# Performance work log

Hardware: AMD Instinct MI355X
Metric: run time of the kernel (lower is better)

The kernel has to match this reference:

```python
import jax, jax.numpy as jnp
import numpy as np

B, C, H, W_ = 4, 256, 64, 64
INTER = 128

def conv1x1(x, w, b):
    # x: [B,C,H,W], w: [O,C], b: [O] -> [B,O,H,W]
    return jnp.einsum('bchw,oc->bohw', x, w) + b[None, :, None, None]

def setup_inputs() -> dict:
    key = jax.random.key(0)
    ks = jax.random.split(key, 5)
    s_in = 1.0 / np.sqrt(C)
    s_mid = 1.0 / np.sqrt(INTER)
    return {
        'x': jax.random.normal(ks[0], (B, C, H, W_), dtype=jnp.float32),
        'w_g': jax.random.normal(ks[1], (INTER, C), dtype=jnp.float32) * s_in,
        'b_g': jnp.zeros((INTER,), dtype=jnp.float32),
        'w_theta': jax.random.normal(ks[2], (INTER, C), dtype=jnp.float32) * s_in,
        'b_theta': jnp.zeros((INTER,), dtype=jnp.float32),
        'w_phi': jax.random.normal(ks[3], (INTER, C), dtype=jnp.float32) * s_in,
        'b_phi': jnp.zeros((INTER,), dtype=jnp.float32),
        'w_out': jax.random.normal(ks[4], (C, INTER), dtype=jnp.float32) * s_mid,
        'b_out': jnp.zeros((C,), dtype=jnp.float32),
    }

def reference(x, w_g, b_g, w_theta, b_theta, w_phi, b_phi, w_out, b_out):
    b, c, h, w = x.shape
    n = h * w
    # 1x1 conv projections, flatten spatial dims to N tokens
    g_x = conv1x1(x, w_g, b_g).reshape(b, INTER, n).transpose(0, 2, 1)      # [B,N,I]
    theta_x = conv1x1(x, w_theta, b_theta).reshape(b, INTER, n).transpose(0, 2, 1)  # [B,N,I]
    phi_x = conv1x1(x, w_phi, b_phi).reshape(b, INTER, n)                   # [B,I,N]
    f = jnp.einsum('bni,bim->bnm', theta_x, phi_x)                          # [B,N,N]
    f_div_C = jax.nn.softmax(f, axis=-1)
    y = jnp.einsum('bnm,bmi->bni', f_div_C, g_x)                            # [B,N,I]
    y = y.transpose(0, 2, 1).reshape(b, INTER, h, w)
    W_y = conv1x1(y, w_out, b_out)                                          # [B,C,H,W]
    return W_y + x
```

## Files before the change

kernel.cpp:

```cpp
#include <hip/hip_runtime.h>

#define BB 4
#define CC 256
#define NN 4096
#define II 128
#define NSPLIT 4
#define KVH (NN / NSPLIT)
#define NT (KVH / 64)
#define LOG2E 1.4426950408889634f

typedef float f32x4 __attribute__((ext_vector_type(4)));
typedef _Float16 f16x8 __attribute__((ext_vector_type(8)));

static __device__ __forceinline__ unsigned short f2h(float f) {
    _Float16 h = (_Float16)f;
    return __builtin_bit_cast(unsigned short, h);
}
static __device__ __forceinline__ float h2f(unsigned short s) {
    return (float)__builtin_bit_cast(_Float16, s);
}
static __device__ __forceinline__ unsigned int pack2h(float a, float b) {
    return (unsigned int)f2h(a) | ((unsigned int)f2h(b) << 16);
}
static __device__ __forceinline__ unsigned int cvt2h(float a, float b) {
    return __builtin_bit_cast(unsigned int, __builtin_amdgcn_cvt_pkrtz(a, b));
}
#define M3(a, b, c) fmaxf(fmaxf((a), (b)), (c))

__global__ __launch_bounds__(256) void proj_kernel(
    const float* __restrict__ x,
    const float* __restrict__ w_th, const float* __restrict__ b_th,
    const float* __restrict__ w_ph, const float* __restrict__ b_ph,
    const float* __restrict__ w_g,  const float* __restrict__ b_g,
    const float* __restrict__ w_out,
    unsigned short* __restrict__ Qb, unsigned short* __restrict__ Kb,
    unsigned short* __restrict__ Vt, unsigned short* __restrict__ Wo)
{
    __shared__ char lds[24576];
    unsigned short* wl = (unsigned short*)lds;
    unsigned short* xl = (unsigned short*)(lds + 16384);

    int tid = threadIdx.x;
    int w = tid >> 6, l = tid & 63, g = l >> 4, cl = l & 15;
    int mat = blockIdx.z, b = blockIdx.y, n0 = blockIdx.x * 64;
    const float* wp = (mat == 0) ? w_th : (mat == 1) ? w_ph : w_g;
    const float* bp = (mat == 0) ? b_th : (mat == 1) ? b_ph : b_g;

    f32x4 acc[2][4];
    #pragma unroll
    for (int it = 0; it < 2; ++it)
        #pragma unroll
        for (int nt = 0; nt < 4; ++nt) acc[it][nt] = (f32x4){0.f, 0.f, 0.f, 0.f};

    const float* xb = x + (size_t)b * CC * NN;
    int c2 = tid >> 3, nch = tid & 7;

    for (int c0 = 0; c0 < CC; c0 += 64) {
        __syncthreads();
        #pragma unroll
        for (int r = 0; r < 4; ++r) {
            int idx = r * 256 + tid;
            int row = idx >> 3, ch = idx & 7;
            const float* src = wp + row * CC + c0 + ch * 8;
            float4 a = *(const float4*)src;
            float4 bq = *(const float4*)(src + 4);
            union { unsigned int u[4]; uint4 q; } pk;
            pk.u[0] = pack2h(a.x, a.y);  pk.u[1] = pack2h(a.z, a.w);
            pk.u[2] = pack2h(bq.x, bq.y); pk.u[3] = pack2h(bq.z, bq.w);
            *(uint4*)((char*)wl + row * 128 + ((ch ^ (row & 7)) << 4)) = pk.q;
        }
        {
            const float* xsrc = xb + (size_t)(c0 + c2 * 2) * NN + n0 + nch * 8;
            float4 x00 = *(const float4*)xsrc;
            float4 x01 = *(const float4*)(xsrc + 4);
            float4 x10 = *(const float4*)(xsrc + NN);
            float4 x11 = *(const float4*)(xsrc + NN + 4);
            float lo[8] = {x00.x, x00.y, x00.z, x00.w, x01.x, x01.y, x01.z, x01.w};
            float hi[8] = {x10.x, x10.y, x10.z, x10.w, x11.x, x11.y, x11.z, x11.w};
            #pragma unroll
            for (int t = 0; t < 8; ++t) {
                int n = nch * 8 + t;
                *(unsigned int*)((char*)xl + n * 128 + ((c2 * 4) ^ ((n & 7) << 4))) = pack2h(lo[t], hi[t]);
            }
        }
        __syncthreads();
        #pragma unroll
        for (int kc = 0; kc < 2; ++kc) {
            f16x8 af[2], bf[4];
            #pragma unroll
            for (int it = 0; it < 2; ++it) {
                int row = w * 32 + it * 16 + cl;
                af[it] = *(const f16x8*)((const char*)wl + row * 128 + (((kc * 4 + g) ^ (row & 7)) << 4));
            }
            #pragma unroll
            for (int nt = 0; nt < 4; ++nt) {
                int row = nt * 16 + cl;
                bf[nt] = *(const f16x8*)((const char*)xl + row * 128 + (((kc * 4 + g) ^ (row & 7)) << 4));
            }
            #pragma unroll
            for (int it = 0; it < 2; ++it)
                #pragma unroll
                for (int nt = 0; nt < 4; ++nt)
                    acc[it][nt] = __builtin_amdgcn_mfma_f32_16x16x32_f16(af[it], bf[nt], acc[it][nt], 0, 0, 0);
        }
    }

    float bv[2][4];
    #pragma unroll
    for (int it = 0; it < 2; ++it)
        #pragma unroll
        for (int r = 0; r < 4; ++r) bv[it][r] = bp[w * 32 + it * 16 + 4 * g + r];
    float scale = (mat == 0) ? LOG2E : 1.0f;

    __syncthreads();
    if (mat < 2) {
        unsigned short* pk = (unsigned short*)lds;
        #pragma unroll
        for (int it = 0; it < 2; ++it)
            #pragma unroll
            for (int nt = 0; nt < 4; ++nt)
                #pragma unroll
                for (int r = 0; r < 4; r += 2) {
                    int n = nt * 16 + cl;
                    int i = w * 32 + it * 16 + 4 * g + r;
                    unsigned int v = pack2h((acc[it][nt][r] + bv[it][r]) * scale,
                                            (acc[it][nt][r + 1] + bv[it][r + 1]) * scale);
                    *(unsigned int*)((char*)pk + n * 256 + ((i * 2) ^ ((n & 7) << 4))) = v;
                }
        __syncthreads();
        unsigned short* out = (mat == 0) ? Qb : Kb;
        #pragma unroll
        for (int r = 0; r < 4; ++r) {
            int idx = r * 256 + tid;
            int n = idx >> 4, seg = idx & 15;
            uint4 q = *(const uint4*)((const char*)pk + n * 256 + ((seg << 4) ^ ((n & 7) << 4)));
            *(uint4*)(out + (size_t)(b * NN + n0 + n) * II + seg * 8) = q;
        }
    } else {
        unsigned short* pk = (unsigned short*)lds;
        #pragma unroll
        for (int it = 0; it < 2; ++it)
            #pragma unroll
            for (int nt = 0; nt < 4; ++nt)
                #pragma unroll
                for (int r = 0; r < 4; ++r) {
                    int i = w * 32 + it * 16 + 4 * g + r;
                    int n = nt * 16 + cl;
                    *(unsigned short*)((char*)pk + i * 128 + ((n * 2) ^ ((i & 7) << 4))) =
                        f2h(acc[it][nt][r] + bv[it][r]);
                }
        __syncthreads();
        #pragma unroll
        for (int r = 0; r < 4; ++r) {
            int idx = r * 256 + tid;
            int i = idx >> 3, seg = idx & 7;
            uint4 q = *(const uint4*)((const char*)pk + i * 128 + ((seg << 4) ^ ((i & 7) << 4)));
            *(uint4*)(Vt + (size_t)(b * II + i) * NN + n0 + seg * 8) = q;
        }
        if (blockIdx.x == 0) {
            #pragma unroll
            for (int r = 0; r < 16; ++r) {
                int idx = (r * 256 + tid) * 8;
                float4 a = *(const float4*)(w_out + idx);
                float4 b4 = *(const float4*)(w_out + idx + 4);
                union { unsigned int u[4]; uint4 q; } pw;
                pw.u[0] = pack2h(a.x, a.y);   pw.u[1] = pack2h(a.z, a.w);
                pw.u[2] = pack2h(b4.x, b4.y); pw.u[3] = pack2h(b4.z, b4.w);
                *(uint4*)&Wo[idx] = pw.q;
            }
        }
    }
}

__global__ __launch_bounds__(256, 2) void attn_kernel(
    const unsigned short* __restrict__ Qb,
    const unsigned short* __restrict__ Kb,
    const unsigned short* __restrict__ Vb,
    unsigned short* __restrict__ Yp,
    float2* __restrict__ ML)
{
    __shared__ unsigned short Ks[2][64 * 128];
    __shared__ unsigned short Vs[2][128 * 64];

    int tid = threadIdx.x;
    int w = tid >> 6, l = tid & 63, g = l >> 4, cl = l & 15;
    int id = blockIdx.x;
    int comb = (id & 7) * 2 + ((id >> 3) & 1);
    int b = comb >> 2, sp = comb & 3, qt = id >> 4;
    int qr0 = qt * 128;
    int m_base = sp * KVH;

    f16x8 qa0[4], qa1[4];
    {
        const unsigned short* qrow0 = Qb + (size_t)(b * NN + qr0 + w * 32 + cl) * II;
        const unsigned short* qrow1 = qrow0 + 16 * II;
        #pragma unroll
        for (int kc = 0; kc < 4; ++kc) {
            qa0[kc] = *(const f16x8*)(qrow0 + kc * 32 + g * 8);
            qa1[kc] = *(const f16x8*)(qrow1 + kc * 32 + g * 8);
        }
    }
    const f16x8 onesv = {(_Float16)1.f, (_Float16)1.f, (_Float16)1.f, (_Float16)1.f,
                         (_Float16)1.f, (_Float16)1.f, (_Float16)1.f, (_Float16)1.f};

    f32x4 yacc0[8], yacc1[8], lacc0, lacc1;
    #pragma unroll
    for (int it = 0; it < 8; ++it) {
        yacc0[it] = (f32x4){0.f, 0.f, 0.f, 0.f};
        yacc1[it] = (f32x4){0.f, 0.f, 0.f, 0.f};
    }
    lacc0 = (f32x4){0.f, 0.f, 0.f, 0.f};
    lacc1 = (f32x4){0.f, 0.f, 0.f, 0.f};
    float mrun0 = -1e30f, mrun1 = -1e30f;

    const unsigned short* kb = Kb + (size_t)(b * NN + m_base) * II;
    const unsigned short* vb = Vb + (size_t)b * II * NN + m_base;
    int krow = tid >> 4, kch = tid & 15;
    int vrow = tid >> 3, vch = tid & 7;
    int kswz = (kch ^ (krow & 7)) << 4;
    int vsw = (vrow & 7) << 4;
    int vc0 = ((vch >> 2) * 32 + (vch & 1) * 16 + ((vch >> 1) & 1) * 4) * 2;

    uint4 k0, k1, k2, k3, v0, v1, v2, v3;
    k0 = *(const uint4*)(kb + (size_t)(krow) * II + kch * 8);
    k1 = *(const uint4*)(kb + (size_t)(16 + krow) * II + kch * 8);
    k2 = *(const uint4*)(kb + (size_t)(32 + krow) * II + kch * 8);
    k3 = *(const uint4*)(kb + (size_t)(48 + krow) * II + kch * 8);
    v0 = *(const uint4*)(vb + (size_t)(vrow) * NN + vch * 8);
    v1 = *(const uint4*)(vb + (size_t)(32 + vrow) * NN + vch * 8);
    v2 = *(const uint4*)(vb + (size_t)(64 + vrow) * NN + vch * 8);
    v3 = *(const uint4*)(vb + (size_t)(96 + vrow) * NN + vch * 8);
    {
        *(uint4*)((char*)Ks[0] + (krow) * 256 + kswz) = k0;
        *(uint4*)((char*)Ks[0] + (16 + krow) * 256 + kswz) = k1;
        *(uint4*)((char*)Ks[0] + (32 + krow) * 256 + kswz) = k2;
        *(uint4*)((char*)Ks[0] + (48 + krow) * 256 + kswz) = k3;
        uint2 lo, hi;
        lo.x = v0.x; lo.y = v0.y; hi.x = v0.z; hi.y = v0.w;
        *(uint2*)((char*)Vs[0] + (vrow) * 128 + (vc0 ^ vsw)) = lo;
        *(uint2*)((char*)Vs[0] + (vrow) * 128 + ((vc0 + 16) ^ vsw)) = hi;
        lo.x = v1.x; lo.y = v1.y; hi.x = v1.z; hi.y = v1.w;
        *(uint2*)((char*)Vs[0] + (32 + vrow) * 128 + (vc0 ^ vsw)) = lo;
        *(uint2*)((char*)Vs[0] + (32 + vrow) * 128 + ((vc0 + 16) ^ vsw)) = hi;
        lo.x = v2.x; lo.y = v2.y; hi.x = v2.z; hi.y = v2.w;
        *(uint2*)((char*)Vs[0] + (64 + vrow) * 128 + (vc0 ^ vsw)) = lo;
        *(uint2*)((char*)Vs[0] + (64 + vrow) * 128 + ((vc0 + 16) ^ vsw)) = hi;
        lo.x = v3.x; lo.y = v3.y; hi.x = v3.z; hi.y = v3.w;
        *(uint2*)((char*)Vs[0] + (96 + vrow) * 128 + (vc0 ^ vsw)) = lo;
        *(uint2*)((char*)Vs[0] + (96 + vrow) * 128 + ((vc0 + 16) ^ vsw)) = hi;
    }

    for (int t = 0; t < NT; ++t) {
        __syncthreads();
        const unsigned short* ksb = Ks[t & 1];
        const unsigned short* vsb = Vs[t & 1];
        unsigned short* kw = Ks[(t + 1) & 1];
        unsigned short* vw = Vs[(t + 1) & 1];
        bool more = (t + 1 < NT);
        if (more) {
            const unsigned short* kp = kb + (size_t)(t + 1) * 64 * II;
            const unsigned short* vp = vb + (size_t)(t + 1) * 64;
            k0 = *(const uint4*)(kp + (size_t)(krow) * II + kch * 8);
            k1 = *(const uint4*)(kp + (size_t)(16 + krow) * II + kch * 8);
            k2 = *(const uint4*)(kp + (size_t)(32 + krow) * II + kch * 8);
            k3 = *(const uint4*)(kp + (size_t)(48 + krow) * II + kch * 8);
            v0 = *(const uint4*)(vp + (size_t)(vrow) * NN + vch * 8);
            v1 = *(const uint4*)(vp + (size_t)(32 + vrow) * NN + vch * 8);
            v2 = *(const uint4*)(vp + (size_t)(64 + vrow) * NN + vch * 8);
            v3 = *(const uint4*)(vp + (size_t)(96 + vrow) * NN + vch * 8);
        }

        f32x4 s0[4], s1[4];
        #pragma unroll
        for (int mt = 0; mt < 4; ++mt) {
            s0[mt] = (f32x4){0.f, 0.f, 0.f, 0.f};
            s1[mt] = (f32x4){0.f, 0.f, 0.f, 0.f};
        }
        __builtin_amdgcn_s_setprio(1);
        #pragma unroll
        for (int mt = 0; mt < 4; ++mt) {
            int row = mt * 16 + cl;
            #pragma unroll
            for (int kc = 0; kc < 4; ++kc) {
                f16x8 kf = *(const f16x8*)((const char*)ksb + row * 256 + (((kc * 4 + g) ^ (row & 7)) << 4));
                s0[mt] = __builtin_amdgcn_mfma_f32_16x16x32_f16(kf, qa0[kc], s0[mt], 0, 0, 0);
                s1[mt] = __builtin_amdgcn_mfma_f32_16x16x32_f16(kf, qa1[kc], s1[mt], 0, 0, 0);
            }
        }
        __builtin_amdgcn_s_setprio(0);

        if (more) {
            *(uint4*)((char*)kw + (krow) * 256 + kswz) = k0;
            *(uint4*)((char*)kw + (16 + krow) * 256 + kswz) = k1;
            *(uint4*)((char*)kw + (32 + krow) * 256 + kswz) = k2;
            *(uint4*)((char*)kw + (48 + krow) * 256 + kswz) = k3;
        }

        union { unsigned int u[4]; f16x8 v; } pb00, pb01, pb10, pb11;
        {
            float t0 = M3(s0[0][0], s0[0][1], s0[0][2]);
            float t1 = M3(s0[0][3], s0[1][0], s0[1][1]);
            float t2 = M3(s0[1][2], s0[1][3], s0[2][0]);
            float t3 = M3(s0[2][1], s0[2][2], s0[2][3]);
            float t4 = M3(s0[3][0], s0[3][1], s0[3][2]);
            float tmax = fmaxf(M3(t0, t1, t2), M3(t3, t4, s0[3][3]));
            tmax = fmaxf(tmax, __shfl_xor(tmax, 16));
            tmax = fmaxf(tmax, __shfl_xor(tmax, 32));
            if (!__all(tmax <= mrun0 + 8.0f)) {
                float mnew = fmaxf(mrun0, tmax);
                float corr = exp2f(mrun0 - mnew);
                mrun0 = mnew;
                #pragma unroll
                for (int it = 0; it < 8; ++it)
                    #pragma unroll
                    for (int r = 0; r < 4; ++r) yacc0[it][r] *= corr;
                #pragma unroll
                for (int r = 0; r < 4; ++r) lacc0[r] *= corr;
            }
            #pragma unroll
            for (int mt = 0; mt < 4; ++mt) {
                unsigned int ua = cvt2h(exp2f(s0[mt][0] - mrun0), exp2f(s0[mt][1] - mrun0));
                unsigned int ub = cvt2h(exp2f(s0[mt][2] - mrun0), exp2f(s0[mt][3] - mrun0));
                if (mt < 2) { pb00.u[mt * 2] = ua; pb00.u[mt * 2 + 1] = ub; }
                else        { pb01.u[(mt - 2) * 2] = ua; pb01.u[(mt - 2) * 2 + 1] = ub; }
            }
        }
        {
            float t0 = M3(s1[0][0], s1[0][1], s1[0][2]);
            float t1 = M3(s1[0][3], s1[1][0], s1[1][1]);
            float t2 = M3(s1[1][2], s1[1][3], s1[2][0]);
            float t3 = M3(s1[2][1], s1[2][2], s1[2][3]);
            float t4 = M3(s1[3][0], s1[3][1], s1[3][2]);
            float tmax = fmaxf(M3(t0, t1, t2), M3(t3, t4, s1[3][3]));
            tmax = fmaxf(tmax, __shfl_xor(tmax, 16));
            tmax = fmaxf(tmax, __shfl_xor(tmax, 32));
            if (!__all(tmax <= mrun1 + 8.0f)) {
                float mnew = fmaxf(mrun1, tmax);
                float corr = exp2f(mrun1 - mnew);
                mrun1 = mnew;
                #pragma unroll
                for (int it = 0; it < 8; ++it)
                    #pragma unroll
                    for (int r = 0; r < 4; ++r) yacc1[it][r] *= corr;
                #pragma unroll
                for (int r = 0; r < 4; ++r) lacc1[r] *= corr;
            }
            #pragma unroll
            for (int mt = 0; mt < 4; ++mt) {
                unsigned int ua = cvt2h(exp2f(s1[mt][0] - mrun1), exp2f(s1[mt][1] - mrun1));
                unsigned int ub = cvt2h(exp2f(s1[mt][2] - mrun1), exp2f(s1[mt][3] - mrun1));
                if (mt < 2) { pb10.u[mt * 2] = ua; pb10.u[mt * 2 + 1] = ub; }
                else        { pb11.u[(mt - 2) * 2] = ua; pb11.u[(mt - 2) * 2 + 1] = ub; }
            }
        }

        if (more) {
            uint2 lo, hi;
            lo.x = v0.x; lo.y = v0.y; hi.x = v0.z; hi.y = v0.w;
            *(uint2*)((char*)vw + (vrow) * 128 + (vc0 ^ vsw)) = lo;
            *(uint2*)((char*)vw + (vrow) * 128 + ((vc0 + 16) ^ vsw)) = hi;
            lo.x = v1.x; lo.y = v1.y; hi.x = v1.z; hi.y = v1.w;
            *(uint2*)((char*)vw + (32 + vrow) * 128 + (vc0 ^ vsw)) = lo;
            *(uint2*)((char*)vw + (32 + vrow) * 128 + ((vc0 + 16) ^ vsw)) = hi;
            lo.x = v2.x; lo.y = v2.y; hi.x = v2.z; hi.y = v2.w;
            *(uint2*)((char*)vw + (64 + vrow) * 128 + (vc0 ^ vsw)) = lo;
            *(uint2*)((char*)vw + (64 + vrow) * 128 + ((vc0 + 16) ^ vsw)) = hi;
            lo.x = v3.x; lo.y = v3.y; hi.x = v3.z; hi.y = v3.w;
            *(uint2*)((char*)vw + (96 + vrow) * 128 + (vc0 ^ vsw)) = lo;
            *(uint2*)((char*)vw + (96 + vrow) * 128 + ((vc0 + 16) ^ vsw)) = hi;
        }

        __builtin_amdgcn_s_setprio(1);
        lacc0 = __builtin_amdgcn_mfma_f32_16x16x32_f16(onesv, pb00.v, lacc0, 0, 0, 0);
        lacc0 = __builtin_amdgcn_mfma_f32_16x16x32_f16(onesv, pb01.v, lacc0, 0, 0, 0);
        lacc1 = __builtin_amdgcn_mfma_f32_16x16x32_f16(onesv, pb10.v, lacc1, 0, 0, 0);
        lacc1 = __builtin_amdgcn_mfma_f32_16x16x32_f16(onesv, pb11.v, lacc1, 0, 0, 0);
        #pragma unroll
        for (int it = 0; it < 8; ++it) {
            int row = it * 16 + cl;
            f16x8 vf0 = *(const f16x8*)((const char*)vsb + row * 128 + ((g ^ (row & 7)) << 4));
            f16x8 vf1 = *(const f16x8*)((const char*)vsb + row * 128 + (((4 + g) ^ (row & 7)) << 4));
            yacc0[it] = __builtin_amdgcn_mfma_f32_16x16x32_f16(vf0, pb00.v, yacc0[it], 0, 0, 0);
            yacc0[it] = __builtin_amdgcn_mfma_f32_16x16x32_f16(vf1, pb01.v, yacc0[it], 0, 0, 0);
            yacc1[it] = __builtin_amdgcn_mfma_f32_16x16x32_f16(vf0, pb10.v, yacc1[it], 0, 0, 0);
            yacc1[it] = __builtin_amdgcn_mfma_f32_16x16x32_f16(vf1, pb11.v, yacc1[it], 0, 0, 0);
        }
        __builtin_amdgcn_s_setprio(0);
    }

    __syncthreads();

    unsigned short* ys = &Ks[0][w * 2048];
    size_t rowbase0 = (size_t)((sp * BB + b) * NN + qr0 + w * 32);
    int prow = l >> 2;
    {
        float rl = 1.0f / lacc0[0];
        #pragma unroll
        for (int it = 0; it < 8; ++it)
            #pragma unroll
            for (int r = 0; r < 4; r += 2) {
                int i = it * 16 + 4 * g + r;
                *(unsigned int*)((char*)ys + cl * 256 + ((i * 2) ^ ((cl & 7) << 4))) =
                    pack2h(yacc0[it][r] * rl, yacc0[it][r + 1] * rl);
            }
        #pragma unroll
        for (int c = 0; c < 4; ++c) {
            int seg = c * 4 + (l & 3);
            uint4 q = *(const uint4*)((const char*)ys + prow * 256 + ((seg << 4) ^ ((prow & 7) << 4)));
            *(uint4*)(Yp + (rowbase0 + prow) * II + seg * 8) = q;
        }
    }
    {
        float rl = 1.0f / lacc1[0];
        #pragma unroll
        for (int it = 0; it < 8; ++it)
            #pragma unroll
            for (int r = 0; r < 4; r += 2) {
                int i = it * 16 + 4 * g + r;
                *(unsigned int*)((char*)ys + cl * 256 + ((i * 2) ^ ((cl & 7) << 4))) =
                    pack2h(yacc1[it][r] * rl, yacc1[it][r + 1] * rl);
            }
        #pragma unroll
        for (int c = 0; c < 4; ++c) {
            int seg = c * 4 + (l & 3);
            uint4 q = *(const uint4*)((const char*)ys + prow * 256 + ((seg << 4) ^ ((prow & 7) << 4)));
            *(uint4*)(Yp + (rowbase0 + 16 + prow) * II + seg * 8) = q;
        }
    }
    if (l < 16) {
        float2 v; v.x = mrun0; v.y = lacc0[0];
        ML[rowbase0 + l] = v;
    } else if (l < 32) {
        float2 v; v.x = mrun1; v.y = lacc1[0];
        ML[rowbase0 + 16 + (l - 16)] = v;
    }
}

__global__ __launch_bounds__(256) void combine_kernel(
    const unsigned short* __restrict__ Yp, const float2* __restrict__ ML,
    const unsigned short* __restrict__ Wo, const float* __restrict__ b_out,
    const float* __restrict__ x, float* __restrict__ out)
{
    __shared__ unsigned short Ys[4][16 * 128];

    int tid = threadIdx.x;
    int w = tid >> 6, l = tid & 63, g = l >> 4, cl = l & 15;
    int qt = blockIdx.x, b = blockIdx.y;
    int n = qt * 32 + (w & 1) * 16 + cl;
    int ct0 = (w >> 1) * 8;

    float ms[NSPLIT], ls[NSPLIT], wgt[NSPLIT];
    float M = -1e30f;
    #pragma unroll
    for (int s = 0; s < NSPLIT; ++s) {
        float2 ml = ML[(size_t)(s * BB + b) * NN + n];
        ms[s] = ml.x; ls[s] = ml.y;
        M = fmaxf(M, ml.x);
    }
    float wsum = 0.f;
    #pragma unroll
    for (int s = 0; s < NSPLIT; ++s) { wgt[s] = exp2f(ms[s] - M) * ls[s]; wsum += wgt[s]; }
    float rd = 1.0f / wsum;
    #pragma unroll
    for (int s = 0; s < NSPLIT; ++s) wgt[s] *= rd;

    unsigned short* ys = Ys[w];
    #pragma unroll
    for (int j = 0; j < 4; ++j) {
        float acc[8];
        #pragma unroll
        for (int e = 0; e < 8; ++e) acc[e] = 0.f;
        #pragma unroll
        for (int s = 0; s < NSPLIT; ++s) {
            union { unsigned short s16[8]; uint4 q; } a;
            a.q = *(const uint4*)(Yp + ((size_t)(s * BB + b) * NN + n) * II + g * 32 + j * 8);
            #pragma unroll
            for (int e = 0; e < 8; ++e) acc[e] += wgt[s] * h2f(a.s16[e]);
        }
        union { unsigned int u[4]; uint4 q; } o;
        #pragma unroll
        for (int e = 0; e < 4; ++e) o.u[e] = pack2h(acc[e * 2], acc[e * 2 + 1]);
        *(uint4*)((char*)ys + cl * 256 + (((g * 4 + j) ^ (cl & 7)) << 4)) = o.q;
    }

    f32x4 zero4 = {0.f, 0.f, 0.f, 0.f};
    f16x8 yf[4];
    #pragma unroll
    for (int kc = 0; kc < 4; ++kc)
        yf[kc] = *(const f16x8*)((const char*)ys + cl * 256 + (((kc * 4 + g) ^ (cl & 7)) << 4));
    for (int ct = ct0; ct < ct0 + 8; ++ct) {
        f32x4 oa = zero4;
        #pragma unroll
        for (int kc = 0; kc < 4; ++kc) {
            f16x8 wf = *(const f16x8*)(Wo + (ct * 16 + cl) * II + kc * 32 + g * 8);
            oa = __builtin_amdgcn_mfma_f32_16x16x32_f16(wf, yf[kc], oa, 0, 0, 0);
        }
        #pragma unroll
        for (int r = 0; r < 4; ++r) {
            int c = ct * 16 + 4 * g + r;
            size_t off = (size_t)(b * CC + c) * NN + n;
            out[off] = oa[r] + b_out[c] + x[off];
        }
    }
}

extern "C" void kernel_launch(void* const* d_in, const int* in_sizes, int n_in,
                              void* d_out, int out_size, void* d_ws, size_t ws_size,
                              hipStream_t stream) {
    const float* x     = (const float*)d_in[0];
    const float* w_g   = (const float*)d_in[1];
    const float* b_g   = (const float*)d_in[2];
    const float* w_th  = (const float*)d_in[3];
    const float* b_th  = (const float*)d_in[4];
    const float* w_ph  = (const float*)d_in[5];
    const float* b_ph  = (const float*)d_in[6];
    const float* w_out = (const float*)d_in[7];
    const float* b_o   = (const float*)d_in[8];
    float* out = (float*)d_out;

    const size_t SZ = (size_t)BB * NN * II;
    unsigned short* Qb = (unsigned short*)d_ws;
    unsigned short* Kb = Qb + SZ;
    unsigned short* Vt = Kb + SZ;
    unsigned short* Wo = Vt + SZ;
    unsigned short* Yp = Wo + (size_t)CC * II;
    float2*         ML = (float2*)(Yp + (size_t)NSPLIT * SZ);

    proj_kernel<<<dim3(NN / 64, BB, 3), dim3(256), 0, stream>>>(
        x, w_th, b_th, w_ph, b_ph, w_g, b_g, w_out, Qb, Kb, Vt, Wo);
    attn_kernel<<<dim3(NSPLIT * BB * (NN / 128)), dim3(256), 0, stream>>>(
        Qb, Kb, Vt, Yp, ML);
    combine_kernel<<<dim3(NN / 32, BB), dim3(256), 0, stream>>>(Yp, ML, Wo, b_o, x, out);
}
```

Baseline: 92.41 us.

## Fuse Q/K/V projections into one block sharing staged x tile; retile combine

The projection kernel now computes theta, phi and g for a 32-token tile in a single block, loading and converting x to fp16 in LDS once instead of once per matrix. Weights for all three matrices are streamed per 32-channel chunk, and outputs are staged in LDS before coalesced stores. The combine kernel is retiled to 16 tokens per block with each wave handling 4 channel tiles. This trades triple x reads for more weight rereads, larger LDS use and more redundant split-merge work in combine.

```diff
diff --git a/kernel.cpp b/kernel.cpp
--- a/kernel.cpp
+++ b/kernel.cpp
@@ -36,138 +36,145 @@
     unsigned short* __restrict__ Qb, unsigned short* __restrict__ Kb,
     unsigned short* __restrict__ Vt, unsigned short* __restrict__ Wo)
 {
-    __shared__ char lds[24576];
-    unsigned short* wl = (unsigned short*)lds;
-    unsigned short* xl = (unsigned short*)(lds + 16384);
+    __shared__ char lds[40960];
 
     int tid = threadIdx.x;
     int w = tid >> 6, l = tid & 63, g = l >> 4, cl = l & 15;
-    int mat = blockIdx.z, b = blockIdx.y, n0 = blockIdx.x * 64;
-    const float* wp = (mat == 0) ? w_th : (mat == 1) ? w_ph : w_g;
-    const float* bp = (mat == 0) ? b_th : (mat == 1) ? b_ph : b_g;
-
-    f32x4 acc[2][4];
-    #pragma unroll
-    for (int it = 0; it < 2; ++it)
-        #pragma unroll
-        for (int nt = 0; nt < 4; ++nt) acc[it][nt] = (f32x4){0.f, 0.f, 0.f, 0.f};
-
+    int b = blockIdx.y, n0 = blockIdx.x * 32;
+    const float* wp0 = w_th; const float* wp1 = w_ph; const float* wp2 = w_g;
     const float* xb = x + (size_t)b * CC * NN;
-    int c2 = tid >> 3, nch = tid & 7;
-
-    for (int c0 = 0; c0 < CC; c0 += 64) {
-        __syncthreads();
-        #pragma unroll
-        for (int r = 0; r < 4; ++r) {
-            int idx = r * 256 + tid;
-            int row = idx >> 3, ch = idx & 7;
-            const float* src = wp + row * CC + c0 + ch * 8;
-            float4 a = *(const float4*)src;
-            float4 bq = *(const float4*)(src + 4);
-            union { unsigned int u[4]; uint4 q; } pk;
-            pk.u[0] = pack2h(a.x, a.y);  pk.u[1] = pack2h(a.z, a.w);
-            pk.u[2] = pack2h(bq.x, bq.y); pk.u[3] = pack2h(bq.z, bq.w);
-            *(uint4*)((char*)wl + row * 128 + ((ch ^ (row & 7)) << 4)) = pk.q;
-        }
-        {
-            const float* xsrc = xb + (size_t)(c0 + c2 * 2) * NN + n0 + nch * 8;
-            float4 x00 = *(const float4*)xsrc;
-            float4 x01 = *(const float4*)(xsrc + 4);
-            float4 x10 = *(const float4*)(xsrc + NN);
-            float4 x11 = *(const float4*)(xsrc + NN + 4);
-            float lo[8] = {x00.x, x00.y, x00.z, x00.w, x01.x, x01.y, x01.z, x01.w};
-            float hi[8] = {x10.x, x10.y, x10.z, x10.w, x11.x, x11.y, x11.z, x11.w};
+
+    {
+        int cp = tid >> 2, nch = tid & 3;
+        #pragma unroll
+        for (int h = 0; h < 2; ++h) {
+            int cpp = h * 64 + cp;
+            const float* xs = xb + (size_t)(2 * cpp) * NN + n0 + nch * 8;
+            float4 a0 = *(const float4*)xs;
+            float4 a1 = *(const float4*)(xs + 4);
+            float4 b0 = *(const float4*)(xs + NN);
+            float4 b1 = *(const float4*)(xs + NN + 4);
+            float lo[8] = {a0.x, a0.y, a0.z, a0.w, a1.x, a1.y, a1.z, a1.w};
+            float hi[8] = {b0.x, b0.y, b0.z, b0.w, b1.x, b1.y, b1.z, b1.w};
             #pragma unroll
             for (int t = 0; t < 8; ++t) {
                 int n = nch * 8 + t;
-                *(unsigned int*)((char*)xl + n * 128 + ((c2 * 4) ^ ((n & 7) << 4))) = pack2h(lo[t], hi[t]);
-            }
-        }
+                *(unsigned int*)(lds + n * 512 + ((cpp * 4) ^ ((n & 7) << 4))) = pack2h(lo[t], hi[t]);
+            }
+        }
+    }
+
+    f32x4 acc[3][2][2];
+    #pragma unroll
+    for (int m = 0; m < 3; ++m)
+        #pragma unroll
+        for (int it = 0; it < 2; ++it)
+            #pragma unroll
+            for (int nt = 0; nt < 2; ++nt) acc[m][it][nt] = (f32x4){0.f, 0.f, 0.f, 0.f};
+
+    for (int c0 = 0; c0 < CC; c0 += 32) {
         __syncthreads();
         #pragma unroll
-        for (int kc = 0; kc < 2; ++kc) {
-            f16x8 af[2], bf[4];
+        for (int r = 0; r < 6; ++r) {
+            const int mat = r >> 1;
+            int u = (r & 1) * 256 + tid;
+            int ir = u >> 2, ch = u & 3;
+            const float* wsrc = (mat == 0 ? wp0 : mat == 1 ? wp1 : wp2) + ir * CC + c0 + ch * 8;
+            float4 a = *(const float4*)wsrc;
+            float4 bq = *(const float4*)(wsrc + 4);
+            union { unsigned int uu[4]; uint4 q; } pk;
+            pk.uu[0] = pack2h(a.x, a.y);   pk.uu[1] = pack2h(a.z, a.w);
+            pk.uu[2] = pack2h(bq.x, bq.y); pk.uu[3] = pack2h(bq.z, bq.w);
+            *(uint4*)(lds + 16384 + mat * 8192 + ir * 64 + ((ch * 16) ^ ((ir & 3) << 4))) = pk.q;
+        }
+        __syncthreads();
+        f16x8 bf[2];
+        #pragma unroll
+        for (int nt = 0; nt < 2; ++nt) {
+            int n = nt * 16 + cl;
+            bf[nt] = *(const f16x8*)(lds + n * 512 + ((c0 * 2 + g * 16) ^ ((n & 7) << 4)));
+        }
+        #pragma unroll
+        for (int m = 0; m < 3; ++m) {
+            f16x8 af[2];
             #pragma unroll
             for (int it = 0; it < 2; ++it) {
-                int row = w * 32 + it * 16 + cl;
-                af[it] = *(const f16x8*)((const char*)wl + row * 128 + (((kc * 4 + g) ^ (row & 7)) << 4));
-            }
-            #pragma unroll
-            for (int nt = 0; nt < 4; ++nt) {
-                int row = nt * 16 + cl;
-                bf[nt] = *(const f16x8*)((const char*)xl + row * 128 + (((kc * 4 + g) ^ (row & 7)) << 4));
+                int i = w * 32 + it * 16 + cl;
+                af[it] = *(const f16x8*)(lds + 16384 + m * 8192 + i * 64 + ((g * 16) ^ ((i & 3) << 4)));
             }
             #pragma unroll
             for (int it = 0; it < 2; ++it)
                 #pragma unroll
-                for (int nt = 0; nt < 4; ++nt)
-                    acc[it][nt] = __builtin_amdgcn_mfma_f32_16x16x32_f16(af[it], bf[nt], acc[it][nt], 0, 0, 0);
-        }
-    }
-
-    float bv[2][4];
-    #pragma unroll
-    for (int it = 0; it < 2; ++it)
-        #pragma unroll
-        for (int r = 0; r < 4; ++r) bv[it][r] = bp[w * 32 + it * 16 + 4 * g + r];
-    float scale = (mat == 0) ? LOG2E : 1.0f;
+                for (int nt = 0; nt < 2; ++nt)
+                    acc[m][it][nt] = __builtin_amdgcn_mfma_f32_16x16x32_f16(af[it], bf[nt], acc[m][it][nt], 0, 0, 0);
+        }
+    }
+
+    float bv[3][2][4];
+    #pragma unroll
+    for (int m = 0; m < 3; ++m) {
+        const float* bp = (m == 0) ? b_th : (m == 1) ? b_ph : b_g;
+        #pragma unroll
+        for (int it = 0; it < 2; ++it)
+            #pragma unroll
+            for (int r = 0; r < 4; ++r) bv[m][it][r] = bp[w * 32 + it * 16 + 4 * g + r];
+    }
 
     __syncthreads();
-    if (mat < 2) {
-        unsigned short* pk = (unsigned short*)lds;
+    #pragma unroll
+    for (int m = 0; m < 2; ++m) {
+        float scale = (m == 0) ? LOG2E : 1.0f;
+        char* pk = lds + m * 8192;
         #pragma unroll
         for (int it = 0; it < 2; ++it)
             #pragma unroll
-            for (int nt = 0; nt < 4; ++nt)
+            for (int nt = 0; nt < 2; ++nt)
                 #pragma unroll
                 for (int r = 0; r < 4; r += 2) {
                     int n = nt * 16 + cl;
                     int i = w * 32 + it * 16 + 4 * g + r;
-                    unsigned int v = pack2h((acc[it][nt][r] + bv[it][r]) * scale,
-                                            (acc[it][nt][r + 1] + bv[it][r + 1]) * scale);
-                    *(unsigned int*)((char*)pk + n * 256 + ((i * 2) ^ ((n & 7) << 4))) = v;
+                    unsigned int v = pack2h((acc[m][it][nt][r] + bv[m][it][r]) * scale,
+                                            (acc[m][it][nt][r + 1] + bv[m][it][r + 1]) * scale);
+                    *(unsigned int*)(pk + n * 256 + ((i * 2) ^ ((n & 7) << 4))) = v;
                 }
-        __syncthreads();
-        unsigned short* out = (mat == 0) ? Qb : Kb;
-        #pragma unroll
-        for (int r = 0; r < 4; ++r) {
-            int idx = r * 256 + tid;
-            int n = idx >> 4, seg = idx & 15;
-            uint4 q = *(const uint4*)((const char*)pk + n * 256 + ((seg << 4) ^ ((n & 7) << 4)));
-            *(uint4*)(out + (size_t)(b * NN + n0 + n) * II + seg * 8) = q;
-        }
-    } else {
-        unsigned short* pk = (unsigned short*)lds;
+    }
+    {
+        char* pk = lds + 16384;
         #pragma unroll
         for (int it = 0; it < 2; ++it)
             #pragma unroll
-            for (int nt = 0; nt < 4; ++nt)
+            for (int nt = 0; nt < 2; ++nt)
                 #pragma unroll
                 for (int r = 0; r < 4; ++r) {
                     int i = w * 32 + it * 16 + 4 * g + r;
                     int n = nt * 16 + cl;
-                    *(unsigned short*)((char*)pk + i * 128 + ((n * 2) ^ ((i & 7) << 4))) =
-                        f2h(acc[it][nt][r] + bv[it][r]);
+                    *(unsigned short*)(pk + i * 64 + ((n * 2) ^ ((i & 3) << 4))) =
+                        f2h(acc[2][it][nt][r] + bv[2][it][r]);
                 }
-        __syncthreads();
-        #pragma unroll
-        for (int r = 0; r < 4; ++r) {
-            int idx = r * 256 + tid;
-            int i = idx >> 3, seg = idx & 7;
-            uint4 q = *(const uint4*)((const char*)pk + i * 128 + ((seg << 4) ^ ((i & 7) << 4)));
-            *(uint4*)(Vt + (size_t)(b * II + i) * NN + n0 + seg * 8) = q;
-        }
-        if (blockIdx.x == 0) {
-            #pragma unroll
-            for (int r = 0; r < 16; ++r) {
-                int idx = (r * 256 + tid) * 8;
-                float4 a = *(const float4*)(w_out + idx);
-                float4 b4 = *(const float4*)(w_out + idx + 4);
-                union { unsigned int u[4]; uint4 q; } pw;
-                pw.u[0] = pack2h(a.x, a.y);   pw.u[1] = pack2h(a.z, a.w);
-                pw.u[2] = pack2h(b4.x, b4.y); pw.u[3] = pack2h(b4.z, b4.w);
-                *(uint4*)&Wo[idx] = pw.q;
-            }
+    }
+    __syncthreads();
+    #pragma unroll
+    for (int r2 = 0; r2 < 2; ++r2) {
+        int u = r2 * 256 + tid;
+        int n = u >> 4, seg = u & 15;
+        uint4 q0 = *(const uint4*)(lds + n * 256 + ((seg * 16) ^ ((n & 7) << 4)));
+        *(uint4*)(Qb + (size_t)(b * NN + n0 + n) * II + seg * 8) = q0;
+        uint4 q1 = *(const uint4*)(lds + 8192 + n * 256 + ((seg * 16) ^ ((n & 7) << 4)));
+        *(uint4*)(Kb + (size_t)(b * NN + n0 + n) * II + seg * 8) = q1;
+        int i = u >> 2, ch = u & 3;
+        uint4 q2 = *(const uint4*)(lds + 16384 + i * 64 + ((ch * 16) ^ ((i & 3) << 4)));
+        *(uint4*)(Vt + (size_t)(b * II + i) * NN + n0 + ch * 8) = q2;
+    }
+    if (blockIdx.x == 0 && b == 0) {
+        #pragma unroll
+        for (int r = 0; r < 16; ++r) {
+            int idx = (r * 256 + tid) * 8;
+            float4 a = *(const float4*)(w_out + idx);
+            float4 b4 = *(const float4*)(w_out + idx + 4);
+            union { unsigned int uu[4]; uint4 q; } pw;
+            pw.uu[0] = pack2h(a.x, a.y);   pw.uu[1] = pack2h(a.z, a.w);
+            pw.uu[2] = pack2h(b4.x, b4.y); pw.uu[3] = pack2h(b4.z, b4.w);
+            *(uint4*)&Wo[idx] = pw.q;
         }
     }
 }
@@ -446,8 +453,8 @@
     int tid = threadIdx.x;
     int w = tid >> 6, l = tid & 63, g = l >> 4, cl = l & 15;
     int qt = blockIdx.x, b = blockIdx.y;
-    int n = qt * 32 + (w & 1) * 16 + cl;
-    int ct0 = (w >> 1) * 8;
+    int n = qt * 16 + cl;
+    int ct0 = w * 4;
 
     float ms[NSPLIT], ls[NSPLIT], wgt[NSPLIT];
     float M = -1e30f;
@@ -488,7 +495,8 @@
     #pragma unroll
     for (int kc = 0; kc < 4; ++kc)
         yf[kc] = *(const f16x8*)((const char*)ys + cl * 256 + (((kc * 4 + g) ^ (cl & 7)) << 4));
-    for (int ct = ct0; ct < ct0 + 8; ++ct) {
+    #pragma unroll
+    for (int ct = ct0; ct < ct0 + 4; ++ct) {
         f32x4 oa = zero4;
         #pragma unroll
         for (int kc = 0; kc < 4; ++kc) {
@@ -526,9 +534,9 @@
     unsigned short* Yp = Wo + (size_t)CC * II;
     float2*         ML = (float2*)(Yp + (size_t)NSPLIT * SZ);
 
-    proj_kernel<<<dim3(NN / 64, BB, 3), dim3(256), 0, stream>>>(
+    proj_kernel<<<dim3(NN / 32, BB), dim3(256), 0, stream>>>(
         x, w_th, b_th, w_ph, b_ph, w_g, b_g, w_out, Qb, Kb, Vt, Wo);
     attn_kernel<<<dim3(NSPLIT * BB * (NN / 128)), dim3(256), 0, stream>>>(
         Qb, Kb, Vt, Yp, ML);
-    combine_kernel<<<dim3(NN / 32, BB), dim3(256), 0, stream>>>(Yp, ML, Wo, b_o, x, out);
-}
+    combine_kernel<<<dim3(NN / 16, BB), dim3(256), 0, stream>>>(Yp, ML, Wo, b_o, x, out);
+}
```

Result: slower. 94.91 us (+2.7%).
